# Optimization experiments

Hardware: AMD Instinct MI355X
Metric: run time of the kernel (lower is better)

## Reference

```python
import jax, jax.numpy as jnp
import numpy as np

SOS_IDX = 1  # letter2index['<sos>']
NEG_INF = -1e9

def _lstm_cell(x, h, c, W_ih, W_hh, b_ih, b_hh):
    # PyTorch LSTMCell gate order: i, f, g, o
    gates = x @ W_ih.T + h @ W_hh.T + b_ih + b_hh
    i, f, g, o = jnp.split(gates, 4, axis=-1)
    i = jax.nn.sigmoid(i); f = jax.nn.sigmoid(f)
    g = jnp.tanh(g); o = jax.nn.sigmoid(o)
    c_new = f * c + i * g
    h_new = o * jnp.tanh(c_new)
    return h_new, c_new

def setup_inputs() -> dict:
    k = jax.random.key(0)
    ks = jax.random.split(k, 16)
    N, T, L = 32, 512, 128
    V = 8000; E = 256; H = 1024; KS = 128; VS = 128
    s = 0.05
    inp = {}
    inp['key'] = jax.random.normal(ks[0], (N, T, KS), jnp.float32)
    inp['values'] = jax.random.normal(ks[1], (N, T, VS), jnp.float32)
    inp['encoder_lens'] = jax.random.randint(ks[2], (N,), 1, T + 1, jnp.int32)
    inp['text'] = jax.random.randint(ks[3], (N, L), 0, V)
    inp['emb'] = jax.random.normal(ks[4], (V, E), jnp.float32) * s
    inp['emb'] = inp['emb'].at[0].set(0.0)  # padding_idx=0
    inp['W_ih1'] = jax.random.normal(ks[5], (4 * H, E + VS), jnp.float32) * s
    inp['W_hh1'] = jax.random.normal(ks[6], (4 * H, H), jnp.float32) * s
    inp['b_ih1'] = jnp.zeros((4 * H,), jnp.float32)
    inp['b_hh1'] = jnp.zeros((4 * H,), jnp.float32)
    inp['W_ih2'] = jax.random.normal(ks[7], (4 * KS, H), jnp.float32) * s
    inp['W_hh2'] = jax.random.normal(ks[8], (4 * KS, KS), jnp.float32) * s
    inp['b_ih2'] = jnp.zeros((4 * KS,), jnp.float32)
    inp['b_hh2'] = jnp.zeros((4 * KS,), jnp.float32)
    inp['W_out'] = jax.random.normal(ks[9], (V, KS + VS), jnp.float32) * s
    inp['b_out'] = jnp.zeros((V,), jnp.float32)
    return inp

def reference(key, values, encoder_lens, text, emb, W_ih1, W_hh1, b_ih1, b_hh1,
              W_ih2, W_hh2, b_ih2, b_hh2, W_out, b_out):
    N, T_enc, _ = key.shape
    H = W_hh1.shape[1]
    K = W_hh2.shape[1]
    # Teacher forcing (rate=0 -> always): step 0 uses <sos>, step i uses text[:, i-1]
    emb_seq = emb[text]                                   # [N, L, E]
    sos = jnp.broadcast_to(emb[SOS_IDX], (N, emb.shape[1]))
    xs = jnp.concatenate([sos[:, None, :], emb_seq[:, :-1, :]], axis=1)
    xs = jnp.swapaxes(xs, 0, 1)                           # [L, N, E]
    mask = jnp.arange(T_enc)[None, :] >= encoder_lens[:, None]  # [N, T]
    carry0 = (jnp.zeros((N, H), key.dtype), jnp.zeros((N, H), key.dtype),
              jnp.zeros((N, K), key.dtype), jnp.zeros((N, K), key.dtype),
              values[:, 0, :])

    def step(carry, x):
        h1, c1, h2, c2, ctx = carry
        inp = jnp.concatenate([x, ctx], axis=1)
        h1, c1 = _lstm_cell(inp, h1, c1, W_ih1, W_hh1, b_ih1, b_hh1)
        h2, c2 = _lstm_cell(h1, h2, c2, W_ih2, W_hh2, b_ih2, b_hh2)
        energy = jnp.einsum('ntk,nk->nt', key, h2)        # bmm(key, query)
        energy = jnp.where(mask, NEG_INF, energy)
        attn = jax.nn.softmax(energy, axis=1)
        ctx = jnp.einsum('nt,ntv->nv', attn, values)
        pred = jnp.concatenate([h2, ctx], axis=1) @ W_out.T + b_out
        return (h1, c1, h2, c2, ctx), pred

    _, preds = jax.lax.scan(step, carry0, xs)             # [L, N, vocab]
    return jnp.swapaxes(preds, 0, 1)                      # [N, L, vocab]
```

## Files before the change

### kernel.cpp

```cpp
#include <hip/hip_runtime.h>

typedef unsigned short u16;
typedef unsigned int u32;
typedef __attribute__((ext_vector_type(8))) short short8;
typedef __attribute__((ext_vector_type(4))) float f32x4;

#define NB 32
#define TE 512
#define LD 128

__device__ __forceinline__ float bfl(u32 u){ return __uint_as_float(u << 16); }
__device__ __forceinline__ float bfh(u32 u){ return __uint_as_float(u & 0xffff0000u); }
__device__ __forceinline__ float bf1(u16 v){ return __uint_as_float(((u32)v) << 16); }
__device__ __forceinline__ u16 f2bf(float f){
  u32 x = __float_as_uint(f);
  return (u16)((x + 0x7fffu + ((x >> 16) & 1u)) >> 16);
}
__device__ __forceinline__ float sigf(float x){ return 1.0f / (1.0f + __expf(-x)); }

__global__ void k_prep(
    const float* __restrict__ Wih1, const float* __restrict__ Whh1,
    const float* __restrict__ bih1, const float* __restrict__ bhh1,
    const float* __restrict__ Wih2, const float* __restrict__ Whh2,
    const float* __restrict__ bih2, const float* __restrict__ bhh2,
    u16* __restrict__ w1hi, u16* __restrict__ w1lo,
    u16* __restrict__ w2hi, u16* __restrict__ w2lo,
    float* __restrict__ bias1, float* __restrict__ bias2)
{
  int idx = blockIdx.x * 256 + threadIdx.x;
  if (idx < 5767168){
    int j = idx / 1408, c = idx - j * 1408;
    float v = (c < 384) ? Wih1[(size_t)j * 384 + c] : Whh1[(size_t)j * 1024 + (c - 384)];
    u16 h = f2bf(v);
    w1hi[idx] = h;
    w1lo[idx] = f2bf(v - bf1(h));
    return;
  }
  idx -= 5767168;
  if (idx < 589824){
    int j = idx / 1152, c = idx - j * 1152;
    float v = (c < 1024) ? Wih2[(size_t)j * 1024 + c] : Whh2[(size_t)j * 128 + (c - 1024)];
    u16 h = f2bf(v);
    w2hi[idx] = h;
    w2lo[idx] = f2bf(v - bf1(h));
    return;
  }
  idx -= 589824;
  if (idx < 4096){ bias1[idx] = bih1[idx] + bhh1[idx]; return; }
  idx -= 4096;
  if (idx < 512){ bias2[idx] = bih2[idx] + bhh2[idx]; }
}

__global__ void k_init(float* __restrict__ c1a, float* __restrict__ c2,
                       u16* __restrict__ xb, u16* __restrict__ xb2,
                       const float* __restrict__ emb, const float* __restrict__ values)
{
  int idx = blockIdx.x * 256 + threadIdx.x;
  if (idx < 32768){ c1a[idx] = 0.0f; return; }
  idx -= 32768;
  if (idx < 4096){ c2[idx] = 0.0f; return; }
  idx -= 4096;
  if (idx < 45056){
    int n = idx / 1408, c = idx - n * 1408;
    u16 v = 0;
    if (c < 256)      v = f2bf(emb[256 + c]);
    else if (c < 384) v = f2bf(values[((size_t)n * TE) * 128 + (c - 256)]);
    xb[idx] = v;
    return;
  }
  idx -= 45056;
  if (idx < 36864) xb2[idx] = 0;
}

__global__ __launch_bounds__(256) void k_gates1(
    const u16* __restrict__ xb, const u16* __restrict__ w1hi, const u16* __restrict__ w1lo,
    float* __restrict__ gp1)
{
  int lane = threadIdx.x & 63, wid = threadIdx.x >> 6;
  int u0 = blockIdx.x * 64 + wid * 16;
  int kp = blockIdx.y;
  int r = lane & 15, kb = lane >> 4;
  const short8* wh = (const short8*)w1hi + (size_t)(u0 + r) * 176 + kp * 44 + kb;
  const short8* wl = (const short8*)w1lo + (size_t)(u0 + r) * 176 + kp * 44 + kb;
  const short8* xa = (const short8*)xb + (size_t)r * 176 + kp * 44 + kb;
  const short8* xc = xa + 16 * 176;
  f32x4 acc0 = {0.f,0.f,0.f,0.f}, acc1 = {0.f,0.f,0.f,0.f};
  #pragma unroll
  for (int s = 0; s < 11; s++){
    short8 bh = wh[4*s], bl = wl[4*s];
    short8 a0 = xa[4*s], a1 = xc[4*s];
    acc0 = __builtin_amdgcn_mfma_f32_16x16x32_bf16(a0, bh, acc0, 0, 0, 0);
    acc1 = __builtin_amdgcn_mfma_f32_16x16x32_bf16(a1, bh, acc1, 0, 0, 0);
    acc0 = __builtin_amdgcn_mfma_f32_16x16x32_bf16(a0, bl, acc0, 0, 0, 0);
    acc1 = __builtin_amdgcn_mfma_f32_16x16x32_bf16(a1, bl, acc1, 0, 0, 0);
  }
  int j = u0 + r;
  float* g = gp1 + (size_t)kp * (NB * 4096);
  #pragma unroll
  for (int q = 0; q < 4; q++){
    int n = kb * 4 + q;
    g[(size_t)n * 4096 + j] = acc0[q];
    g[(size_t)(n + 16) * 4096 + j] = acc1[q];
  }
}

__global__ __launch_bounds__(256) void k_cell1(
    const float* __restrict__ gp1, const float* __restrict__ bias1,
    const float* __restrict__ c1in, float* __restrict__ c1out,
    u16* __restrict__ xb, u16* __restrict__ xb2)
{
  int idx = blockIdx.x * 256 + threadIdx.x;
  int n = idx >> 10, u = idx & 1023;
  float g[4];
  #pragma unroll
  for (int e = 0; e < 4; e++){
    int j = e * 1024 + u;
    float s = bias1[j];
    #pragma unroll
    for (int p = 0; p < 4; p++) s += gp1[((size_t)p * NB + n) * 4096 + j];
    g[e] = s;
  }
  float gi = sigf(g[0]), gf = sigf(g[1]), gg = tanhf(g[2]), go = sigf(g[3]);
  float cn = gf * c1in[idx] + gi * gg;
  c1out[idx] = cn;
  float hn = go * tanhf(cn);
  u16 hb = f2bf(hn);
  xb[(size_t)n * 1408 + 384 + u] = hb;
  xb2[(size_t)n * 1152 + u] = hb;
}

__global__ __launch_bounds__(256) void k_gates2(
    const u16* __restrict__ xb2, const u16* __restrict__ w2hi, const u16* __restrict__ w2lo,
    float* __restrict__ gp2)
{
  int lane = threadIdx.x & 63, wid = threadIdx.x >> 6;
  int u0 = blockIdx.x * 64 + wid * 16;
  int kp = blockIdx.y;
  int r = lane & 15, kb = lane >> 4;
  const short8* wh = (const short8*)w2hi + (size_t)(u0 + r) * 144 + kp * 36 + kb;
  const short8* wl = (const short8*)w2lo + (size_t)(u0 + r) * 144 + kp * 36 + kb;
  const short8* xa = (const short8*)xb2 + (size_t)r * 144 + kp * 36 + kb;
  const short8* xc = xa + 16 * 144;
  f32x4 acc0 = {0.f,0.f,0.f,0.f}, acc1 = {0.f,0.f,0.f,0.f};
  #pragma unroll
  for (int s = 0; s < 9; s++){
    short8 bh = wh[4*s], bl = wl[4*s];
    short8 a0 = xa[4*s], a1 = xc[4*s];
    acc0 = __builtin_amdgcn_mfma_f32_16x16x32_bf16(a0, bh, acc0, 0, 0, 0);
    acc1 = __builtin_amdgcn_mfma_f32_16x16x32_bf16(a1, bh, acc1, 0, 0, 0);
    acc0 = __builtin_amdgcn_mfma_f32_16x16x32_bf16(a0, bl, acc0, 0, 0, 0);
    acc1 = __builtin_amdgcn_mfma_f32_16x16x32_bf16(a1, bl, acc1, 0, 0, 0);
  }
  int j = u0 + r;
  float* g = gp2 + (size_t)kp * (NB * 512);
  #pragma unroll
  for (int q = 0; q < 4; q++){
    int n = kb * 4 + q;
    g[(size_t)n * 512 + j] = acc0[q];
    g[(size_t)(n + 16) * 512 + j] = acc1[q];
  }
}

__global__ __launch_bounds__(512) void k_attn(
    int t, const float* __restrict__ key, const float* __restrict__ values,
    const int* __restrict__ elen, const int* __restrict__ text, const float* __restrict__ emb,
    const float* __restrict__ bias2, const float* __restrict__ gp2,
    float* __restrict__ c2g, u16* __restrict__ xb, u16* __restrict__ xb2,
    u16* __restrict__ aall)
{
  __shared__ float s_h2[128];
  __shared__ float s_e[512];
  __shared__ float s_part[4][128];
  __shared__ float s_red[8];
  __shared__ float s_scal[2];
  int tid = threadIdx.x;
  int n = blockIdx.x;
  if (tid < 128){
    int u = tid;
    float g[4];
    #pragma unroll
    for (int e = 0; e < 4; e++){
      int j = e * 128 + u;
      float s = bias2[j];
      #pragma unroll
      for (int pp = 0; pp < 4; pp++) s += gp2[((size_t)pp * NB + n) * 512 + j];
      g[e] = s;
    }
    float gi = sigf(g[0]), gf = sigf(g[1]), gt = tanhf(g[2]), go = sigf(g[3]);
    float cn = gf * c2g[n * 128 + u] + gi * gt;
    c2g[n * 128 + u] = cn;
    float hn = go * tanhf(cn);
    s_h2[u] = hn;
    u16 hb = f2bf(hn);
    xb2[(size_t)n * 1152 + 1024 + u] = hb;
    aall[((size_t)(t - 1) * NB + n) * 256 + u] = hb;
  } else if (tid < 384){
    int c = tid - 128;
    int tok = text[n * LD + (t - 1)];
    xb[(size_t)n * 1408 + c] = f2bf(emb[(size_t)tok * 256 + c]);
  }
  __syncthreads();
  int el = elen[n];
  const float4* krow = (const float4*)(key + ((size_t)n * TE + tid) * 128);
  float e = 0.0f;
  #pragma unroll 8
  for (int q = 0; q < 32; q++){
    float4 w = krow[q];
    e += w.x*s_h2[4*q+0] + w.y*s_h2[4*q+1] + w.z*s_h2[4*q+2] + w.w*s_h2[4*q+3];
  }
  if (tid >= el) e = -1e9f;
  float m = e;
  for (int off = 32; off > 0; off >>= 1) m = fmaxf(m, __shfl_xor(m, off));
  if ((tid & 63) == 0) s_red[tid >> 6] = m;
  __syncthreads();
  if (tid == 0){
    float mm = s_red[0];
    for (int w = 1; w < 8; w++) mm = fmaxf(mm, s_red[w]);
    s_scal[0] = mm;
  }
  __syncthreads();
  float pr = __expf(e - s_scal[0]);
  s_e[tid] = pr;
  float sm = pr;
  for (int off = 32; off > 0; off >>= 1) sm += __shfl_xor(sm, off);
  if ((tid & 63) == 0) s_red[tid >> 6] = sm;
  __syncthreads();
  if (tid == 0){
    float ss = 0.0f;
    for (int w = 0; w < 8; w++) ss += s_red[w];
    s_scal[1] = ss;
  }
  __syncthreads();
  int v = tid & 127, ch = tid >> 7;
  const float* vb = values + ((size_t)n * TE + ch * 128) * 128 + v;
  float a = 0.0f;
  #pragma unroll 4
  for (int q = 0; q < 128; q++) a += s_e[ch * 128 + q] * vb[(size_t)q * 128];
  s_part[ch][v] = a;
  __syncthreads();
  if (tid < 128){
    float cv = (s_part[0][tid] + s_part[1][tid] + s_part[2][tid] + s_part[3][tid]) / s_scal[1];
    u16 cb = f2bf(cv);
    xb[(size_t)n * 1408 + 256 + tid] = cb;
    aall[((size_t)(t - 1) * NB + n) * 256 + 128 + tid] = cb;
  }
}

__global__ __launch_bounds__(256) void k_out(
    const u16* __restrict__ aall, const float* __restrict__ wout,
    const float* __restrict__ bout, float* __restrict__ out)
{
  __shared__ __align__(16) u16 sA[128 * 136];
  __shared__ __align__(16) u16 sW[80 * 136];
  int tid = threadIdx.x;
  int vt = blockIdx.x, rt = blockIdx.y;
  int v0 = vt * 80, r0 = rt * 128;
  int rg = tid >> 4, vg = tid & 15;
  float acc[8][5];
  #pragma unroll
  for (int i = 0; i < 8; i++)
    #pragma unroll
    for (int j = 0; j < 5; j++) acc[i][j] = 0.0f;
  for (int kc = 0; kc < 2; kc++){
    int k0 = kc * 128;
    __syncthreads();
    for (int i = tid; i < 128 * 128; i += 256){
      int r = i >> 7, c = i & 127;
      sA[r * 136 + c] = aall[((size_t)(r0 + r)) * 256 + k0 + c];
    }
    for (int i = tid; i < 80 * 128; i += 256){
      int r = i >> 7, c = i & 127;
      sW[r * 136 + c] = f2bf(wout[((size_t)(v0 + r)) * 256 + k0 + c]);
    }
    __syncthreads();
    const u16* ap = sA + (rg * 8) * 136;
    const u16* wp = sW + (vg * 5) * 136;
    for (int kp = 0; kp < 64; kp++){
      u32 av[8], wv[5];
      #pragma unroll
      for (int i = 0; i < 8; i++) av[i] = *(const u32*)(ap + i * 136 + 2 * kp);
      #pragma unroll
      for (int j = 0; j < 5; j++) wv[j] = *(const u32*)(wp + j * 136 + 2 * kp);
      float wlo[5], whi[5];
      #pragma unroll
      for (int j = 0; j < 5; j++){ wlo[j] = bfl(wv[j]); whi[j] = bfh(wv[j]); }
      #pragma unroll
      for (int i = 0; i < 8; i++){
        float a0 = bfl(av[i]), a1 = bfh(av[i]);
        #pragma unroll
        for (int j = 0; j < 5; j++) acc[i][j] += a0 * wlo[j] + a1 * whi[j];
      }
    }
  }
  #pragma unroll
  for (int i = 0; i < 8; i++){
    int r = r0 + rg * 8 + i;
    int tt = r >> 5, nn = r & 31;
    size_t ob = ((size_t)nn * LD + tt) * 8000 + v0 + vg * 5;
    #pragma unroll
    for (int j = 0; j < 5; j++){
      out[ob + j] = acc[i][j] + bout[v0 + vg * 5 + j];
    }
  }
}

extern "C" void kernel_launch(void* const* d_in, const int* in_sizes, int n_in,
                              void* d_out, int out_size, void* d_ws, size_t ws_size,
                              hipStream_t stream)
{
  const float* key    = (const float*)d_in[0];
  const float* values = (const float*)d_in[1];
  const int*   elen   = (const int*)d_in[2];
  const int*   text   = (const int*)d_in[3];
  const float* emb    = (const float*)d_in[4];
  const float* Wih1   = (const float*)d_in[5];
  const float* Whh1   = (const float*)d_in[6];
  const float* bih1   = (const float*)d_in[7];
  const float* bhh1   = (const float*)d_in[8];
  const float* Wih2   = (const float*)d_in[9];
  const float* Whh2   = (const float*)d_in[10];
  const float* bih2   = (const float*)d_in[11];
  const float* bhh2   = (const float*)d_in[12];
  const float* Wout   = (const float*)d_in[13];
  const float* bout   = (const float*)d_in[14];
  float* out = (float*)d_out;
  float* ws = (float*)d_ws;

  float* c1a = ws;
  float* c1b = c1a + 32768;
  float* c2  = c1b + 32768;
  u16*  aall = (u16*)(c2 + 4096);

  float* sc = out + 25600000;
  u16* w1hi = (u16*)sc;
  u16* w1lo = w1hi + 5767168;
  u16* w2hi = w1lo + 5767168;
  u16* w2lo = w2hi + 589824;
  u16* xb   = w2lo + 589824;
  u16* xb2  = xb + 45056;
  float* bias1 = (float*)(xb2 + 36864);
  float* bias2 = bias1 + 4096;
  float* gp1   = bias2 + 512;
  float* gp2   = gp1 + 524288;

  k_prep<<<24850, 256, 0, stream>>>(Wih1, Whh1, bih1, bhh1, Wih2, Whh2, bih2, bhh2,
                                    w1hi, w1lo, w2hi, w2lo, bias1, bias2);
  k_init<<<464, 256, 0, stream>>>(c1a, c2, xb, xb2, emb, values);

  for (int t = 0; t < 128; t++){
    if (t > 0)
      k_attn<<<32, 512, 0, stream>>>(t, key, values, elen, text, emb, bias2,
                                     gp2, c2, xb, xb2, aall);
    k_gates1<<<dim3(64, 4), 256, 0, stream>>>(xb, w1hi, w1lo, gp1);
    const float* c1in = (t & 1) ? c1b : c1a;
    float* c1out = (t & 1) ? c1a : c1b;
    k_cell1<<<128, 256, 0, stream>>>(gp1, bias1, c1in, c1out, xb, xb2);
    k_gates2<<<dim3(8, 4), 256, 0, stream>>>(xb2, w2hi, w2lo, gp2);
  }
  k_attn<<<32, 512, 0, stream>>>(128, key, values, elen, text, emb, bias2,
                                 gp2, c2, xb, xb2, aall);
  k_out<<<dim3(100, 32), 256, 0, stream>>>(aall, Wout, bout, out);
}
```

Before: 5.050 ms.

## Fuse recurrent timestep loop into persistent cooperative kernel with grid barriers

Replaces the roughly 512 per-timestep kernel launches (gates1, cell1, gates2, attn) with a single cooperative persistent kernel of 128 blocks. The blocks synchronise through an atomic-counter grid barrier, three barriers per step plus one after init. Layer-1 gates are now computed per block over the full K dimension and fed straight into the cell update through shared memory, which drops the gp1 partial-sum round trip. The x input is double-buffered so that attention can write the next step's input while gates1 still reads the current one. In exchange, each step runs on only 128 blocks with serialized barriers, and blocks 32 to 127 sit idle during the layer-2 and attention phases.

New measurement: 8.883 ms. +75.9%, slower.

```diff
diff --git a/kernel.cpp b/kernel.cpp
--- a/kernel.cpp
+++ b/kernel.cpp
@@ -8,6 +8,7 @@
 #define NB 32
 #define TE 512
 #define LD 128
+#define NBLK 128
 
 __device__ __forceinline__ float bfl(u32 u){ return __uint_as_float(u << 16); }
 __device__ __forceinline__ float bfh(u32 u){ return __uint_as_float(u & 0xffff0000u); }
@@ -17,6 +18,20 @@
   return (u16)((x + 0x7fffu + ((x >> 16) & 1u)) >> 16);
 }
 __device__ __forceinline__ float sigf(float x){ return 1.0f / (1.0f + __expf(-x)); }
+
+__device__ __forceinline__ void gbar(u32* bar, u32* bc){
+  __syncthreads();
+  *bc += 1;
+  if (threadIdx.x == 0){
+    __hip_atomic_fetch_add(bar, 1u, __ATOMIC_RELEASE, __HIP_MEMORY_SCOPE_AGENT);
+    u32 target = *bc * NBLK;
+    while (__hip_atomic_load(bar, __ATOMIC_RELAXED, __HIP_MEMORY_SCOPE_AGENT) < target){
+      __builtin_amdgcn_s_sleep(1);
+    }
+    (void)__hip_atomic_load(bar, __ATOMIC_ACQUIRE, __HIP_MEMORY_SCOPE_AGENT);
+  }
+  __syncthreads();
+}
 
 __global__ void k_prep(
     const float* __restrict__ Wih1, const float* __restrict__ Whh1,
@@ -25,9 +40,11 @@
     const float* __restrict__ bih2, const float* __restrict__ bhh2,
     u16* __restrict__ w1hi, u16* __restrict__ w1lo,
     u16* __restrict__ w2hi, u16* __restrict__ w2lo,
-    float* __restrict__ bias1, float* __restrict__ bias2)
+    float* __restrict__ bias1, float* __restrict__ bias2,
+    u32* __restrict__ bar)
 {
   int idx = blockIdx.x * 256 + threadIdx.x;
+  if (idx == 0) *bar = 0u;
   if (idx < 5767168){
     int j = idx / 1408, c = idx - j * 1408;
     float v = (c < 384) ? Wih1[(size_t)j * 384 + c] : Whh1[(size_t)j * 1024 + (c - 384)];
@@ -51,198 +68,191 @@
   if (idx < 512){ bias2[idx] = bih2[idx] + bhh2[idx]; }
 }
 
-__global__ void k_init(float* __restrict__ c1a, float* __restrict__ c2,
-                       u16* __restrict__ xb, u16* __restrict__ xb2,
-                       const float* __restrict__ emb, const float* __restrict__ values)
+__global__ __launch_bounds__(256) void k_persist(
+    const float* __restrict__ key, const float* __restrict__ values,
+    const int* __restrict__ elen, const int* __restrict__ text,
+    const float* __restrict__ emb,
+    const u16* __restrict__ w1hi, const u16* __restrict__ w1lo,
+    const u16* __restrict__ w2hi, const u16* __restrict__ w2lo,
+    const float* __restrict__ bias1, const float* __restrict__ bias2,
+    u16* __restrict__ xbA, u16* __restrict__ xbB, u16* __restrict__ xb2,
+    float* __restrict__ c1, float* __restrict__ c2,
+    float* __restrict__ gp2f, u16* __restrict__ aall,
+    u32* __restrict__ bar)
 {
-  int idx = blockIdx.x * 256 + threadIdx.x;
-  if (idx < 32768){ c1a[idx] = 0.0f; return; }
-  idx -= 32768;
-  if (idx < 4096){ c2[idx] = 0.0f; return; }
-  idx -= 4096;
-  if (idx < 45056){
-    int n = idx / 1408, c = idx - n * 1408;
-    u16 v = 0;
-    if (c < 256)      v = f2bf(emb[256 + c]);
-    else if (c < 384) v = f2bf(values[((size_t)n * TE) * 128 + (c - 256)]);
-    xb[idx] = v;
-    return;
-  }
-  idx -= 45056;
-  if (idx < 36864) xb2[idx] = 0;
-}
-
-__global__ __launch_bounds__(256) void k_gates1(
-    const u16* __restrict__ xb, const u16* __restrict__ w1hi, const u16* __restrict__ w1lo,
-    float* __restrict__ gp1)
-{
-  int lane = threadIdx.x & 63, wid = threadIdx.x >> 6;
-  int u0 = blockIdx.x * 64 + wid * 16;
-  int kp = blockIdx.y;
-  int r = lane & 15, kb = lane >> 4;
-  const short8* wh = (const short8*)w1hi + (size_t)(u0 + r) * 176 + kp * 44 + kb;
-  const short8* wl = (const short8*)w1lo + (size_t)(u0 + r) * 176 + kp * 44 + kb;
-  const short8* xa = (const short8*)xb + (size_t)r * 176 + kp * 44 + kb;
-  const short8* xc = xa + 16 * 176;
-  f32x4 acc0 = {0.f,0.f,0.f,0.f}, acc1 = {0.f,0.f,0.f,0.f};
-  #pragma unroll
-  for (int s = 0; s < 11; s++){
-    short8 bh = wh[4*s], bl = wl[4*s];
-    short8 a0 = xa[4*s], a1 = xc[4*s];
-    acc0 = __builtin_amdgcn_mfma_f32_16x16x32_bf16(a0, bh, acc0, 0, 0, 0);
-    acc1 = __builtin_amdgcn_mfma_f32_16x16x32_bf16(a1, bh, acc1, 0, 0, 0);
-    acc0 = __builtin_amdgcn_mfma_f32_16x16x32_bf16(a0, bl, acc0, 0, 0, 0);
-    acc1 = __builtin_amdgcn_mfma_f32_16x16x32_bf16(a1, bl, acc1, 0, 0, 0);
-  }
-  int j = u0 + r;
-  float* g = gp1 + (size_t)kp * (NB * 4096);
-  #pragma unroll
-  for (int q = 0; q < 4; q++){
-    int n = kb * 4 + q;
-    g[(size_t)n * 4096 + j] = acc0[q];
-    g[(size_t)(n + 16) * 4096 + j] = acc1[q];
-  }
-}
-
-__global__ __launch_bounds__(256) void k_cell1(
-    const float* __restrict__ gp1, const float* __restrict__ bias1,
-    const float* __restrict__ c1in, float* __restrict__ c1out,
-    u16* __restrict__ xb, u16* __restrict__ xb2)
-{
-  int idx = blockIdx.x * 256 + threadIdx.x;
-  int n = idx >> 10, u = idx & 1023;
-  float g[4];
-  #pragma unroll
-  for (int e = 0; e < 4; e++){
-    int j = e * 1024 + u;
-    float s = bias1[j];
-    #pragma unroll
-    for (int p = 0; p < 4; p++) s += gp1[((size_t)p * NB + n) * 4096 + j];
-    g[e] = s;
-  }
-  float gi = sigf(g[0]), gf = sigf(g[1]), gg = tanhf(g[2]), go = sigf(g[3]);
-  float cn = gf * c1in[idx] + gi * gg;
-  c1out[idx] = cn;
-  float hn = go * tanhf(cn);
-  u16 hb = f2bf(hn);
-  xb[(size_t)n * 1408 + 384 + u] = hb;
-  xb2[(size_t)n * 1152 + u] = hb;
-}
-
-__global__ __launch_bounds__(256) void k_gates2(
-    const u16* __restrict__ xb2, const u16* __restrict__ w2hi, const u16* __restrict__ w2lo,
-    float* __restrict__ gp2)
-{
-  int lane = threadIdx.x & 63, wid = threadIdx.x >> 6;
-  int u0 = blockIdx.x * 64 + wid * 16;
-  int kp = blockIdx.y;
-  int r = lane & 15, kb = lane >> 4;
-  const short8* wh = (const short8*)w2hi + (size_t)(u0 + r) * 144 + kp * 36 + kb;
-  const short8* wl = (const short8*)w2lo + (size_t)(u0 + r) * 144 + kp * 36 + kb;
-  const short8* xa = (const short8*)xb2 + (size_t)r * 144 + kp * 36 + kb;
-  const short8* xc = xa + 16 * 144;
-  f32x4 acc0 = {0.f,0.f,0.f,0.f}, acc1 = {0.f,0.f,0.f,0.f};
-  #pragma unroll
-  for (int s = 0; s < 9; s++){
-    short8 bh = wh[4*s], bl = wl[4*s];
-    short8 a0 = xa[4*s], a1 = xc[4*s];
-    acc0 = __builtin_amdgcn_mfma_f32_16x16x32_bf16(a0, bh, acc0, 0, 0, 0);
-    acc1 = __builtin_amdgcn_mfma_f32_16x16x32_bf16(a1, bh, acc1, 0, 0, 0);
-    acc0 = __builtin_amdgcn_mfma_f32_16x16x32_bf16(a0, bl, acc0, 0, 0, 0);
-    acc1 = __builtin_amdgcn_mfma_f32_16x16x32_bf16(a1, bl, acc1, 0, 0, 0);
-  }
-  int j = u0 + r;
-  float* g = gp2 + (size_t)kp * (NB * 512);
-  #pragma unroll
-  for (int q = 0; q < 4; q++){
-    int n = kb * 4 + q;
-    g[(size_t)n * 512 + j] = acc0[q];
-    g[(size_t)(n + 16) * 512 + j] = acc1[q];
-  }
-}
-
-__global__ __launch_bounds__(512) void k_attn(
-    int t, const float* __restrict__ key, const float* __restrict__ values,
-    const int* __restrict__ elen, const int* __restrict__ text, const float* __restrict__ emb,
-    const float* __restrict__ bias2, const float* __restrict__ gp2,
-    float* __restrict__ c2g, u16* __restrict__ xb, u16* __restrict__ xb2,
-    u16* __restrict__ aall)
-{
+  __shared__ float smem[2048];
   __shared__ float s_h2[128];
-  __shared__ float s_e[512];
-  __shared__ float s_part[4][128];
-  __shared__ float s_red[8];
-  __shared__ float s_scal[2];
+  __shared__ float s_red[4];
   int tid = threadIdx.x;
-  int n = blockIdx.x;
-  if (tid < 128){
-    int u = tid;
-    float g[4];
-    #pragma unroll
-    for (int e = 0; e < 4; e++){
-      int j = e * 128 + u;
-      float s = bias2[j];
-      #pragma unroll
-      for (int pp = 0; pp < 4; pp++) s += gp2[((size_t)pp * NB + n) * 512 + j];
-      g[e] = s;
-    }
-    float gi = sigf(g[0]), gf = sigf(g[1]), gt = tanhf(g[2]), go = sigf(g[3]);
-    float cn = gf * c2g[n * 128 + u] + gi * gt;
-    c2g[n * 128 + u] = cn;
-    float hn = go * tanhf(cn);
-    s_h2[u] = hn;
-    u16 hb = f2bf(hn);
-    xb2[(size_t)n * 1152 + 1024 + u] = hb;
-    aall[((size_t)(t - 1) * NB + n) * 256 + u] = hb;
-  } else if (tid < 384){
-    int c = tid - 128;
-    int tok = text[n * LD + (t - 1)];
-    xb[(size_t)n * 1408 + c] = f2bf(emb[(size_t)tok * 256 + c]);
-  }
-  __syncthreads();
-  int el = elen[n];
-  const float4* krow = (const float4*)(key + ((size_t)n * TE + tid) * 128);
-  float e = 0.0f;
-  #pragma unroll 8
-  for (int q = 0; q < 32; q++){
-    float4 w = krow[q];
-    e += w.x*s_h2[4*q+0] + w.y*s_h2[4*q+1] + w.z*s_h2[4*q+2] + w.w*s_h2[4*q+3];
-  }
-  if (tid >= el) e = -1e9f;
-  float m = e;
-  for (int off = 32; off > 0; off >>= 1) m = fmaxf(m, __shfl_xor(m, off));
-  if ((tid & 63) == 0) s_red[tid >> 6] = m;
-  __syncthreads();
-  if (tid == 0){
-    float mm = s_red[0];
-    for (int w = 1; w < 8; w++) mm = fmaxf(mm, s_red[w]);
-    s_scal[0] = mm;
-  }
-  __syncthreads();
-  float pr = __expf(e - s_scal[0]);
-  s_e[tid] = pr;
-  float sm = pr;
-  for (int off = 32; off > 0; off >>= 1) sm += __shfl_xor(sm, off);
-  if ((tid & 63) == 0) s_red[tid >> 6] = sm;
-  __syncthreads();
-  if (tid == 0){
-    float ss = 0.0f;
-    for (int w = 0; w < 8; w++) ss += s_red[w];
-    s_scal[1] = ss;
-  }
-  __syncthreads();
-  int v = tid & 127, ch = tid >> 7;
-  const float* vb = values + ((size_t)n * TE + ch * 128) * 128 + v;
-  float a = 0.0f;
-  #pragma unroll 4
-  for (int q = 0; q < 128; q++) a += s_e[ch * 128 + q] * vb[(size_t)q * 128];
-  s_part[ch][v] = a;
-  __syncthreads();
-  if (tid < 128){
-    float cv = (s_part[0][tid] + s_part[1][tid] + s_part[2][tid] + s_part[3][tid]) / s_scal[1];
-    u16 cb = f2bf(cv);
-    xb[(size_t)n * 1408 + 256 + tid] = cb;
-    aall[((size_t)(t - 1) * NB + n) * 256 + 128 + tid] = cb;
+  int blk = blockIdx.x;
+  int lane = tid & 63, wid = tid >> 6;
+  u32 bc = 0;
+
+  for (int idx = blk * 256 + tid; idx < 118784; idx += NBLK * 256){
+    int i = idx;
+    if (i < 32768){ c1[i] = 0.0f; continue; }
+    i -= 32768;
+    if (i < 4096){ c2[i] = 0.0f; continue; }
+    i -= 4096;
+    if (i < 45056){
+      int n = i / 1408, c = i - n * 1408;
+      u16 v = 0;
+      if (c < 256)      v = f2bf(emb[256 + c]);
+      else if (c < 384) v = f2bf(values[(size_t)n * TE * 128 + (c - 256)]);
+      xbA[i] = v;
+      continue;
+    }
+    i -= 45056;
+    xb2[i] = 0;
+  }
+  gbar(bar, &bc);
+
+  for (int t = 0; t < 128; t++){
+    const u16* xr = (t & 1) ? xbB : xbA;
+    u16* xw = (t & 1) ? xbA : xbB;
+
+    {
+      int xg = blk & 7, sb = blk >> 3;
+      int g = xg * 8 + (sb >> 1), h = sb & 1;
+      int r = lane & 15, kb = lane >> 4;
+      int row = wid * 1024 + g * 16 + r;
+      const short8* wh = (const short8*)w1hi + (size_t)row * 176 + kb;
+      const short8* wl = (const short8*)w1lo + (size_t)row * 176 + kb;
+      const short8* xa = (const short8*)xr + (size_t)(h * 16 + r) * 176 + kb;
+      f32x4 acc = {0.f, 0.f, 0.f, 0.f};
+      #pragma unroll 4
+      for (int ss = 0; ss < 44; ss++){
+        short8 a  = xa[4 * ss];
+        short8 b0 = wh[4 * ss], b1 = wl[4 * ss];
+        acc = __builtin_amdgcn_mfma_f32_16x16x32_bf16(a, b0, acc, 0, 0, 0);
+        acc = __builtin_amdgcn_mfma_f32_16x16x32_bf16(a, b1, acc, 0, 0, 0);
+      }
+      #pragma unroll
+      for (int q = 0; q < 4; q++){
+        int nl = kb * 4 + q;
+        smem[wid * 256 + nl * 16 + r] = acc[q];
+      }
+      __syncthreads();
+      {
+        int nl = tid >> 4, u = tid & 15;
+        int uu = g * 16 + u;
+        int n = h * 16 + nl;
+        float gi = smem[tid]            + bias1[uu];
+        float gf = smem[256 + tid]      + bias1[1024 + uu];
+        float gg = smem[512 + tid]      + bias1[2048 + uu];
+        float go = smem[768 + tid]      + bias1[3072 + uu];
+        gi = sigf(gi); gf = sigf(gf); gg = tanhf(gg); go = sigf(go);
+        int ci = n * 1024 + uu;
+        float cn = gf * c1[ci] + gi * gg;
+        c1[ci] = cn;
+        float hn = go * tanhf(cn);
+        u16 hb = f2bf(hn);
+        xw[n * 1408 + 384 + uu] = hb;
+        xb2[n * 1152 + uu] = hb;
+      }
+    }
+    gbar(bar, &bc);
+
+    if (blk < 32){
+      int rt = blk;
+      int r = lane & 15, kb = lane >> 4;
+      int row = rt * 16 + r;
+      const short8* wh = (const short8*)w2hi + (size_t)row * 144 + wid * 36 + kb;
+      const short8* wl = (const short8*)w2lo + (size_t)row * 144 + wid * 36 + kb;
+      const short8* xa = (const short8*)xb2 + (size_t)r * 144 + wid * 36 + kb;
+      const short8* xc = xa + 16 * 144;
+      f32x4 acc0 = {0.f,0.f,0.f,0.f}, acc1 = {0.f,0.f,0.f,0.f};
+      #pragma unroll
+      for (int ss = 0; ss < 9; ss++){
+        short8 a0 = xa[4 * ss], a1 = xc[4 * ss];
+        short8 b0 = wh[4 * ss], b1 = wl[4 * ss];
+        acc0 = __builtin_amdgcn_mfma_f32_16x16x32_bf16(a0, b0, acc0, 0, 0, 0);
+        acc1 = __builtin_amdgcn_mfma_f32_16x16x32_bf16(a1, b0, acc1, 0, 0, 0);
+        acc0 = __builtin_amdgcn_mfma_f32_16x16x32_bf16(a0, b1, acc0, 0, 0, 0);
+        acc1 = __builtin_amdgcn_mfma_f32_16x16x32_bf16(a1, b1, acc1, 0, 0, 0);
+      }
+      #pragma unroll
+      for (int q = 0; q < 4; q++){
+        int nl = kb * 4 + q;
+        smem[wid * 512 + nl * 16 + r] = acc0[q];
+        smem[wid * 512 + (nl + 16) * 16 + r] = acc1[q];
+      }
+      __syncthreads();
+      for (int i = tid; i < 512; i += 256){
+        float s = smem[i] + smem[512 + i] + smem[1024 + i] + smem[1536 + i];
+        int n = i >> 4, u = i & 15;
+        gp2f[n * 512 + rt * 16 + u] = s;
+      }
+    }
+    gbar(bar, &bc);
+
+    if (blk < 32){
+      int n = blk;
+      float* s_e = smem;
+      float* s_part = smem + 512;
+      if (tid < 128){
+        int u = tid;
+        float g0 = gp2f[n * 512 + u]       + bias2[u];
+        float g1 = gp2f[n * 512 + 128 + u] + bias2[128 + u];
+        float g2 = gp2f[n * 512 + 256 + u] + bias2[256 + u];
+        float g3 = gp2f[n * 512 + 384 + u] + bias2[384 + u];
+        float gi = sigf(g0), gf = sigf(g1), gt = tanhf(g2), go = sigf(g3);
+        int ci = n * 128 + u;
+        float cn = gf * c2[ci] + gi * gt;
+        c2[ci] = cn;
+        float hn = go * tanhf(cn);
+        s_h2[u] = hn;
+        u16 hb = f2bf(hn);
+        xb2[n * 1152 + 1024 + u] = hb;
+        aall[((size_t)t * NB + n) * 256 + u] = hb;
+      } else {
+        int c = (tid - 128) * 2;
+        int tok = text[n * LD + t];
+        xw[n * 1408 + c]     = f2bf(emb[(size_t)tok * 256 + c]);
+        xw[n * 1408 + c + 1] = f2bf(emb[(size_t)tok * 256 + c + 1]);
+      }
+      __syncthreads();
+      int el = elen[n];
+      float e0 = 0.f, e1 = 0.f;
+      const float4* k0 = (const float4*)(key + ((size_t)n * TE + tid) * 128);
+      const float4* k1 = (const float4*)(key + ((size_t)n * TE + tid + 256) * 128);
+      #pragma unroll 8
+      for (int q = 0; q < 32; q++){
+        float4 wa = k0[q], wb = k1[q];
+        float h0 = s_h2[4*q], h1 = s_h2[4*q+1], h2 = s_h2[4*q+2], h3 = s_h2[4*q+3];
+        e0 += wa.x*h0 + wa.y*h1 + wa.z*h2 + wa.w*h3;
+        e1 += wb.x*h0 + wb.y*h1 + wb.z*h2 + wb.w*h3;
+      }
+      if (tid >= el)       e0 = -1e9f;
+      if (tid + 256 >= el) e1 = -1e9f;
+      float m = fmaxf(e0, e1);
+      for (int off = 32; off > 0; off >>= 1) m = fmaxf(m, __shfl_xor(m, off));
+      if (lane == 0) s_red[wid] = m;
+      __syncthreads();
+      m = fmaxf(fmaxf(s_red[0], s_red[1]), fmaxf(s_red[2], s_red[3]));
+      float p0 = __expf(e0 - m), p1 = __expf(e1 - m);
+      s_e[tid] = p0; s_e[tid + 256] = p1;
+      float sm = p0 + p1;
+      for (int off = 32; off > 0; off >>= 1) sm += __shfl_xor(sm, off);
+      __syncthreads();
+      if (lane == 0) s_red[wid] = sm;
+      __syncthreads();
+      float inv = 1.0f / (s_red[0] + s_red[1] + s_red[2] + s_red[3]);
+      int v = tid & 127, ch = tid >> 7;
+      const float* vb = values + ((size_t)n * TE + ch * 256) * 128 + v;
+      float a = 0.f;
+      #pragma unroll 4
+      for (int q = 0; q < 256; q++) a += s_e[ch * 256 + q] * vb[(size_t)q * 128];
+      s_part[ch * 128 + v] = a;
+      __syncthreads();
+      if (tid < 128){
+        float cv = (s_part[tid] + s_part[128 + tid]) * inv;
+        u16 cb = f2bf(cv);
+        xw[n * 1408 + 256 + tid] = cb;
+        aall[((size_t)t * NB + n) * 256 + 128 + tid] = cb;
+      }
+    }
+    gbar(bar, &bc);
   }
 }
 
@@ -326,38 +336,35 @@
   float* out = (float*)d_out;
   float* ws = (float*)d_ws;
 
-  float* c1a = ws;
-  float* c1b = c1a + 32768;
-  float* c2  = c1b + 32768;
+  float* c1  = ws;
+  float* c2  = c1 + 32768;
   u16*  aall = (u16*)(c2 + 4096);
+  u32*  bar  = (u32*)(aall + 4096 * 256);
 
   float* sc = out + 25600000;
   u16* w1hi = (u16*)sc;
   u16* w1lo = w1hi + 5767168;
   u16* w2hi = w1lo + 5767168;
   u16* w2lo = w2hi + 589824;
-  u16* xb   = w2lo + 589824;
-  u16* xb2  = xb + 45056;
+  u16* xbA  = w2lo + 589824;
+  u16* xbB  = xbA + 45056;
+  u16* xb2  = xbB + 45056;
   float* bias1 = (float*)(xb2 + 36864);
   float* bias2 = bias1 + 4096;
-  float* gp1   = bias2 + 512;
-  float* gp2   = gp1 + 524288;
+  float* gp2f  = bias2 + 512;
 
   k_prep<<<24850, 256, 0, stream>>>(Wih1, Whh1, bih1, bhh1, Wih2, Whh2, bih2, bhh2,
-                                    w1hi, w1lo, w2hi, w2lo, bias1, bias2);
-  k_init<<<464, 256, 0, stream>>>(c1a, c2, xb, xb2, emb, values);
-
-  for (int t = 0; t < 128; t++){
-    if (t > 0)
-      k_attn<<<32, 512, 0, stream>>>(t, key, values, elen, text, emb, bias2,
-                                     gp2, c2, xb, xb2, aall);
-    k_gates1<<<dim3(64, 4), 256, 0, stream>>>(xb, w1hi, w1lo, gp1);
-    const float* c1in = (t & 1) ? c1b : c1a;
-    float* c1out = (t & 1) ? c1a : c1b;
-    k_cell1<<<128, 256, 0, stream>>>(gp1, bias1, c1in, c1out, xb, xb2);
-    k_gates2<<<dim3(8, 4), 256, 0, stream>>>(xb2, w2hi, w2lo, gp2);
-  }
-  k_attn<<<32, 512, 0, stream>>>(128, key, values, elen, text, emb, bias2,
-                                 gp2, c2, xb, xb2, aall);
+                                    w1hi, w1lo, w2hi, w2lo, bias1, bias2, bar);
+
+  void* args[] = {
+    (void*)&key, (void*)&values, (void*)&elen, (void*)&text, (void*)&emb,
+    (void*)&w1hi, (void*)&w1lo, (void*)&w2hi, (void*)&w2lo,
+    (void*)&bias1, (void*)&bias2,
+    (void*)&xbA, (void*)&xbB, (void*)&xb2, (void*)&c1, (void*)&c2,
+    (void*)&gp2f, (void*)&aall, (void*)&bar
+  };
+  hipLaunchCooperativeKernel((const void*)k_persist, dim3(NBLK), dim3(256),
+                             args, 0, stream);
+
   k_out<<<dim3(100, 32), 256, 0, stream>>>(aall, Wout, bout, out);
 }
```
